# Performance work log

Hardware: AMD Instinct MI355X
Metric: run time of the kernel (lower is better)

Reference implementation:

```python
import jax, jax.numpy as jnp
import numpy as np

_FIRST_DECODE_ID = 0  # _T5_DECODER_START_TOKEN_ID
B, L, V = 1, 520, 32128
REVIEW_INDEX = 512
LENIENCY = 2


def setup_inputs() -> dict:
    key = jax.random.key(0)
    k1, k2, k3 = jax.random.split(key, 3)
    target_logits = jax.random.normal(k1, (B, L, V), dtype=jnp.float32)
    probs = jax.random.uniform(k2, (B, L, V), dtype=jnp.float32)
    input_ids = jax.random.randint(k3, (B, L), 0, V, dtype=jnp.int64)
    return {
        "target_logits": target_logits,
        "probs": probs,
        "input_ids": input_ids,
        "review_index": REVIEW_INDEX,
        "leniency": LENIENCY,
    }


def reference(target_logits, probs, input_ids, review_index, leniency):
    r = int(review_index)
    L = input_ids.shape[1]
    K = L - r  # number of draft tokens under review

    target_probs = jax.nn.softmax(target_logits, axis=-1)          # (1, L, V)
    argmax_ids = jnp.argmax(target_probs, axis=-1)                  # (1, L)
    first = jnp.full((1, 1), _FIRST_DECODE_ID, dtype=input_ids.dtype)
    target_ids = jnp.concatenate([first, argmax_ids.astype(input_ids.dtype)], axis=-1)[:, r:]  # (1, K+1)
    target_probs_s = target_probs[:, r - 1:, :]                     # (1, K+1, V)
    probs_new = probs[:, r - 1:, :]                                 # (1, K+1, V)
    draft_ids = input_ids[:, r:]                                    # (1, K)

    # verification flags (fused replacement of the python early-exit loop)
    eq = target_ids[:, :K] == draft_ids                             # (1, K)
    tp = jnp.take_along_axis(target_probs_s[:, :K, :], draft_ids[..., None], axis=-1)[..., 0]
    pp = jnp.take_along_axis(probs_new[:, :K, :], draft_ids[..., None], axis=-1)[..., 0]
    lenient = (leniency > 1) & (tp > pp / jnp.float32(leniency))
    accept = eq | lenient                                           # (1, K)
    # n_match = length of leading run of accepts == match_ct in the loop
    n_match = jnp.sum(jnp.cumprod(accept.astype(jnp.int32), axis=-1))

    # id_res: prefix (r) + accepted drafts (n_match) + 1 bonus target token, padded to r+K+1
    pos = jnp.arange(K + 1)
    draft_pad = jnp.pad(draft_ids, ((0, 0), (0, 1)))                # (1, K+1)
    new_ids = jnp.where(pos < n_match, draft_pad[0],
                        jnp.where(pos == n_match, target_ids[0], 0))
    id_res = jnp.concatenate([input_ids[0, :r], new_ids])[None, :]  # (1, r+K+1)

    # prob_res: probs[:, :r] ++ target_probs of accepted positions, zero-padded to r+K
    mask = (jnp.arange(K) < n_match)[:, None]
    new_probs = jnp.where(mask, target_probs_s[0, :K, :], jnp.float32(0.0))
    prob_res = jnp.concatenate([probs[0, :r, :], new_probs], axis=0)[None]  # (1, r+K, V)

    return id_res, prob_res, n_match
```

## Files before the change

kernel.cpp:

```cpp
#include <hip/hip_runtime.h>
#include <hip/hip_bf16.h>


#define NCHUNK 32
#define BLK 256
#define CP_EPT 8

struct Ws {
    float pmax[16][NCHUNK];
    float psum[16][NCHUNK];
    int   pidx[16][NCHUNK];
    float mx[16];
    float sum[16];
    int   amax[16];
    int   n_match;
};

struct MIS { float m; int i; float s; };

__device__ inline MIS mis_merge(MIS a, MIS b) {
    MIS r;
    r.i = (b.m > a.m || (b.m == a.m && b.i < a.i)) ? b.i : a.i;
    r.m = fmaxf(a.m, b.m);
    r.s = 0.0f;
    if (a.s > 0.0f) r.s += a.s * expf(a.m - r.m);
    if (b.s > 0.0f) r.s += b.s * expf(b.m - r.m);
    return r;
}

typedef float f4u __attribute__((ext_vector_type(4), aligned(4)));

__global__ void fused_copy_stats(const float* __restrict__ logits,
                                 const float* __restrict__ probs,
                                 float* __restrict__ out, Ws* __restrict__ ws,
                                 int V, int row0, long long prob_off,
                                 int nCopyBlocks, int blocksPerRow, int nf4) {
    int t = threadIdx.x;

    if ((int)blockIdx.x < nCopyBlocks) {
        int y   = blockIdx.x / blocksPerRow;
        int sub = blockIdx.x % blocksPerRow;
        const float* src = probs + (size_t)y * V;
        float*       dst = out + prob_off + (size_t)y * V;

        if (sub == 0) {
            if (t < 3)       dst[t] = src[t];
            else if (t == 3) dst[V - 1] = src[V - 1];
        }
        int f0 = sub * (BLK * CP_EPT) + t;
        #pragma unroll
        for (int k = 0; k < CP_EPT; k++) {
            int f = f0 + k * BLK;
            if (f < nf4) {
                f4u v = *reinterpret_cast<const f4u*>(src + 3 + 4 * f);
                *reinterpret_cast<float4*>(dst + 3 + 4 * f) =
                    float4{v.x, v.y, v.z, v.w};
            }
        }
        return;
    }

    int idx = blockIdx.x - nCopyBlocks;
    int ch = idx & (NCHUNK - 1);
    int j  = idx / NCHUNK;
    int chunk_elems = V / NCHUNK;
    int cf4 = chunk_elems / 4;
    int cbase = ch * chunk_elems;
    const float4* row = (const float4*)(logits + (size_t)(row0 + j) * V + cbase);

    float m = -INFINITY, s = 0.0f;
    int   mi = 0x7fffffff;
    for (int f = t; f < cf4; f += BLK) {
        float4 v = row[f];
        float vv[4] = {v.x, v.y, v.z, v.w};
        int c = cbase + f * 4;
        #pragma unroll
        for (int u = 0; u < 4; u++) {
            float x = vv[u];
            if (x > m) { s = s * expf(m - x) + 1.0f; m = x; mi = c + u; }
            else       { s += expf(x - m); }
        }
    }

    __shared__ float sm[BLK];
    __shared__ int   si[BLK];
    __shared__ float ss[BLK];
    sm[t] = m; si[t] = mi; ss[t] = s;
    __syncthreads();
    for (int w = BLK >> 1; w > 0; w >>= 1) {
        if (t < w) {
            MIS a = {sm[t], si[t], ss[t]};
            MIS b = {sm[t + w], si[t + w], ss[t + w]};
            MIS rr = mis_merge(a, b);
            sm[t] = rr.m; si[t] = rr.i; ss[t] = rr.s;
        }
        __syncthreads();
    }
    if (t == 0) {
        ws->pmax[j][ch] = sm[0];
        ws->psum[j][ch] = ss[0];
        ws->pidx[j][ch] = si[0];
    }
}

__global__ void accept_kernel(const float* __restrict__ logits, const float* __restrict__ probs,
                              const int* __restrict__ ids, const int* __restrict__ leniency_p,
                              float* __restrict__ out, Ws* __restrict__ ws,
                              int V, int r, int K, long long out_last) {
    __shared__ int s_draft[16];
    __shared__ int s_acc[16];
    __shared__ int s_nm;
    int t = threadIdx.x;

    if (t <= K) {
        MIS acc = {ws->pmax[t][0], ws->pidx[t][0], ws->psum[t][0]};
        for (int c = 1; c < NCHUNK; c++) {
            MIS b = {ws->pmax[t][c], ws->pidx[t][c], ws->psum[t][c]};
            acc = mis_merge(acc, b);
        }
        ws->mx[t] = acc.m; ws->sum[t] = acc.s; ws->amax[t] = acc.i;
    }
    __syncthreads();

    for (int i = t; i < r; i += blockDim.x) out[i] = (float)ids[i];

    if (t < K) {
        int dj = ids[r + t];
        s_draft[t] = dj;
        size_t rowoff = (size_t)(r - 1 + t) * V;
        float tp = expf(logits[rowoff + dj] - ws->mx[t]) / ws->sum[t];
        float pp = probs[rowoff + dj];
        int   len = *leniency_p;
        bool eq      = (ws->amax[t] == dj);
        bool lenient = (len > 1) && (tp > pp / (float)len);
        s_acc[t] = (eq || lenient) ? 1 : 0;
    }
    __syncthreads();

    if (t == 0) {
        int nm = 0;
        for (int j = 0; j < K; j++) { if (s_acc[j]) nm++; else break; }
        s_nm = nm;
        ws->n_match = nm;
        out[out_last] = (float)nm;
    }
    __syncthreads();

    if (t <= K) {
        int pos = t, nm = s_nm, v;
        if (pos < nm)       v = s_draft[pos];
        else if (pos == nm) v = ws->amax[pos];
        else                v = 0;
        out[r + pos] = (float)v;
    }
}

#define TP_EPT 4

__global__ void tail_probs_kernel(const float* __restrict__ logits,
                                  float* __restrict__ out, const Ws* __restrict__ ws,
                                  int V, int r, long long prob_off) {
    int j = blockIdx.y;
    long long ob = prob_off + (long long)(r + j) * V;
    int c0 = blockIdx.x * (BLK * TP_EPT) + threadIdx.x;
    int nm = ws->n_match;

    if (j < nm) {
        const float* lg = logits + (size_t)(r - 1 + j) * V;
        float m   = ws->mx[j];
        float inv = 1.0f / ws->sum[j];
        #pragma unroll
        for (int k = 0; k < TP_EPT; k++) {
            int c = c0 + k * BLK;
            if (c < V) out[ob + c] = expf(lg[c] - m) * inv;
        }
    } else {
        #pragma unroll
        for (int k = 0; k < TP_EPT; k++) {
            int c = c0 + k * BLK;
            if (c < V) out[ob + c] = 0.0f;
        }
    }
}

extern "C" void kernel_launch(void* const* d_in, const int* in_sizes, int n_in,
                              void* d_out, int out_size, void* d_ws, size_t ws_size,
                              hipStream_t stream) {
    const float* logits     = (const float*)d_in[0];
    const float* probs      = (const float*)d_in[1];
    const int*   ids        = (const int*)d_in[2];
    const int*   leniency_p = (const int*)d_in[4];
    float* out = (float*)d_out;
    Ws*    ws  = (Ws*)d_ws;

    const int L = in_sizes[2];
    const int V = in_sizes[0] / L;
    const int r = 512;
    const int K = L - r;
    const long long prob_off = (long long)r + K + 1;
    const long long out_last = (long long)out_size - 1;

    const int nf4 = (V - 4) / 4;
    const int blocksPerRow = (nf4 + BLK * CP_EPT - 1) / (BLK * CP_EPT);
    const int nCopyBlocks  = r * blocksPerRow;
    const int nStatsBlocks = (K + 1) * NCHUNK;

    fused_copy_stats<<<nCopyBlocks + nStatsBlocks, BLK, 0, stream>>>(
        logits, probs, out, ws, V, r - 1, prob_off, nCopyBlocks, blocksPerRow, nf4);

    accept_kernel<<<1, 512, 0, stream>>>(logits, probs, ids, leniency_p, out, ws,
                                         V, r, K, out_last);

    dim3 g3((V + BLK * TP_EPT - 1) / (BLK * TP_EPT), K, 1);
    tail_probs_kernel<<<g3, BLK, 0, stream>>>(logits, out, ws, V, r, prob_off);
}
```

Measured before the change: 34.79 us.

## Merge accept step into tail kernel and grid-stride the probs copy

The single-block accept kernel is folded into the tail-probs kernel. Every tail block now redundantly merges the per-chunk stats and recomputes n_match in shared memory, which removes one launch and the workspace round trip. The probs copy becomes a flat grid-stride loop over the whole prefix with nontemporal stores and a fixed grid of 2048 blocks, replacing per-row blocks. The tail writes are also vectorized as float4 with nontemporal stores. The cost is redundant per-block reductions, and NSTATS is hardcoded for K=8.

```diff
diff --git a/kernel.cpp b/kernel.cpp
--- a/kernel.cpp
+++ b/kernel.cpp
@@ -4,16 +4,14 @@
 
 #define NCHUNK 32
 #define BLK 256
-#define CP_EPT 8
+#define NSTATS ((8 + 1) * NCHUNK)
+#define GRID1 2048
+#define NCOPY (GRID1 - NSTATS - 1)
 
 struct Ws {
     float pmax[16][NCHUNK];
     float psum[16][NCHUNK];
     int   pidx[16][NCHUNK];
-    float mx[16];
-    float sum[16];
-    int   amax[16];
-    int   n_match;
 };
 
 struct MIS { float m; int i; float s; };
@@ -28,110 +26,114 @@
     return r;
 }
 
+typedef float f4  __attribute__((ext_vector_type(4)));
 typedef float f4u __attribute__((ext_vector_type(4), aligned(4)));
 
 __global__ void fused_copy_stats(const float* __restrict__ logits,
                                  const float* __restrict__ probs,
+                                 const int* __restrict__ ids,
                                  float* __restrict__ out, Ws* __restrict__ ws,
-                                 int V, int row0, long long prob_off,
-                                 int nCopyBlocks, int blocksPerRow, int nf4) {
+                                 int V, int r, long long prob_off, int nf4) {
     int t = threadIdx.x;
-
-    if ((int)blockIdx.x < nCopyBlocks) {
-        int y   = blockIdx.x / blocksPerRow;
-        int sub = blockIdx.x % blocksPerRow;
-        const float* src = probs + (size_t)y * V;
-        float*       dst = out + prob_off + (size_t)y * V;
-
-        if (sub == 0) {
-            if (t < 3)       dst[t] = src[t];
-            else if (t == 3) dst[V - 1] = src[V - 1];
-        }
-        int f0 = sub * (BLK * CP_EPT) + t;
-        #pragma unroll
-        for (int k = 0; k < CP_EPT; k++) {
-            int f = f0 + k * BLK;
-            if (f < nf4) {
-                f4u v = *reinterpret_cast<const f4u*>(src + 3 + 4 * f);
-                *reinterpret_cast<float4*>(dst + 3 + 4 * f) =
-                    float4{v.x, v.y, v.z, v.w};
+    int b = blockIdx.x;
+
+    if (b < NCOPY) {
+        const float* src = probs + 3;
+        float*       dst = out + prob_off + 3;
+        for (int i = b * BLK + t; i < nf4; i += NCOPY * BLK) {
+            f4u v = *reinterpret_cast<const f4u*>(src + 4 * (size_t)i);
+            __builtin_nontemporal_store((f4)v, reinterpret_cast<f4*>(dst + 4 * (size_t)i));
+        }
+        return;
+    }
+
+    if (b < NCOPY + NSTATS) {
+        int idx = b - NCOPY;
+        int ch = idx & (NCHUNK - 1);
+        int j  = idx / NCHUNK;
+        int chunk_elems = V / NCHUNK;
+        int cf4 = chunk_elems / 4;
+        int cbase = ch * chunk_elems;
+        const float4* row = (const float4*)(logits + (size_t)(r - 1 + j) * V + cbase);
+
+        float m = -INFINITY, s = 0.0f;
+        int   mi = 0x7fffffff;
+        for (int f = t; f < cf4; f += BLK) {
+            float4 v = row[f];
+            float vv[4] = {v.x, v.y, v.z, v.w};
+            int c = cbase + f * 4;
+            #pragma unroll
+            for (int u = 0; u < 4; u++) {
+                float x = vv[u];
+                if (x > m) { s = s * expf(m - x) + 1.0f; m = x; mi = c + u; }
+                else       { s += expf(x - m); }
             }
         }
+
+        __shared__ float sm[BLK];
+        __shared__ int   si[BLK];
+        __shared__ float ss[BLK];
+        sm[t] = m; si[t] = mi; ss[t] = s;
+        __syncthreads();
+        for (int w = BLK >> 1; w > 0; w >>= 1) {
+            if (t < w) {
+                MIS a = {sm[t], si[t], ss[t]};
+                MIS bb = {sm[t + w], si[t + w], ss[t + w]};
+                MIS rr = mis_merge(a, bb);
+                sm[t] = rr.m; si[t] = rr.i; ss[t] = rr.s;
+            }
+            __syncthreads();
+        }
+        if (t == 0) {
+            ws->pmax[j][ch] = sm[0];
+            ws->psum[j][ch] = ss[0];
+            ws->pidx[j][ch] = si[0];
+        }
         return;
     }
 
-    int idx = blockIdx.x - nCopyBlocks;
-    int ch = idx & (NCHUNK - 1);
-    int j  = idx / NCHUNK;
-    int chunk_elems = V / NCHUNK;
-    int cf4 = chunk_elems / 4;
-    int cbase = ch * chunk_elems;
-    const float4* row = (const float4*)(logits + (size_t)(row0 + j) * V + cbase);
-
-    float m = -INFINITY, s = 0.0f;
-    int   mi = 0x7fffffff;
-    for (int f = t; f < cf4; f += BLK) {
-        float4 v = row[f];
-        float vv[4] = {v.x, v.y, v.z, v.w};
-        int c = cbase + f * 4;
-        #pragma unroll
-        for (int u = 0; u < 4; u++) {
-            float x = vv[u];
-            if (x > m) { s = s * expf(m - x) + 1.0f; m = x; mi = c + u; }
-            else       { s += expf(x - m); }
-        }
-    }
-
-    __shared__ float sm[BLK];
-    __shared__ int   si[BLK];
-    __shared__ float ss[BLK];
-    sm[t] = m; si[t] = mi; ss[t] = s;
-    __syncthreads();
-    for (int w = BLK >> 1; w > 0; w >>= 1) {
-        if (t < w) {
-            MIS a = {sm[t], si[t], ss[t]};
-            MIS b = {sm[t + w], si[t + w], ss[t + w]};
-            MIS rr = mis_merge(a, b);
-            sm[t] = rr.m; si[t] = rr.i; ss[t] = rr.s;
-        }
-        __syncthreads();
-    }
-    if (t == 0) {
-        ws->pmax[j][ch] = sm[0];
-        ws->psum[j][ch] = ss[0];
-        ws->pidx[j][ch] = si[0];
-    }
-}
-
-__global__ void accept_kernel(const float* __restrict__ logits, const float* __restrict__ probs,
-                              const int* __restrict__ ids, const int* __restrict__ leniency_p,
-                              float* __restrict__ out, Ws* __restrict__ ws,
-                              int V, int r, int K, long long out_last) {
-    __shared__ int s_draft[16];
-    __shared__ int s_acc[16];
-    __shared__ int s_nm;
+    for (int i = t; i < r; i += BLK) out[i] = (float)ids[i];
+    if (t < 3)       out[prob_off + t] = probs[t];
+    else if (t == 3) {
+        long long last = (long long)r * V - 1;
+        out[prob_off + last] = probs[last];
+    }
+}
+
+#define TP_EPT 8
+
+__global__ void tail_kernel(const float* __restrict__ logits, const float* __restrict__ probs,
+                            const int* __restrict__ ids, const int* __restrict__ leniency_p,
+                            float* __restrict__ out, const Ws* __restrict__ ws,
+                            int V, int r, int K, long long prob_off, long long out_last) {
+    __shared__ float s_mx[12];
+    __shared__ float s_sum[12];
+    __shared__ int   s_amax[12];
+    __shared__ int   s_draft[12];
+    __shared__ int   s_acc[12];
+    __shared__ int   s_nm;
     int t = threadIdx.x;
+    int j   = blockIdx.y;
+    int sub = blockIdx.x;
 
     if (t <= K) {
         MIS acc = {ws->pmax[t][0], ws->pidx[t][0], ws->psum[t][0]};
         for (int c = 1; c < NCHUNK; c++) {
-            MIS b = {ws->pmax[t][c], ws->pidx[t][c], ws->psum[t][c]};
-            acc = mis_merge(acc, b);
-        }
-        ws->mx[t] = acc.m; ws->sum[t] = acc.s; ws->amax[t] = acc.i;
+            MIS bb = {ws->pmax[t][c], ws->pidx[t][c], ws->psum[t][c]};
+            acc = mis_merge(acc, bb);
+        }
+        s_mx[t] = acc.m; s_sum[t] = acc.s; s_amax[t] = acc.i;
     }
     __syncthreads();
-
-    for (int i = t; i < r; i += blockDim.x) out[i] = (float)ids[i];
 
     if (t < K) {
         int dj = ids[r + t];
         s_draft[t] = dj;
         size_t rowoff = (size_t)(r - 1 + t) * V;
-        float tp = expf(logits[rowoff + dj] - ws->mx[t]) / ws->sum[t];
+        float tp = expf(logits[rowoff + dj] - s_mx[t]) / s_sum[t];
         float pp = probs[rowoff + dj];
         int   len = *leniency_p;
-        bool eq      = (ws->amax[t] == dj);
+        bool eq      = (s_amax[t] == dj);
         bool lenient = (len > 1) && (tp > pp / (float)len);
         s_acc[t] = (eq || lenient) ? 1 : 0;
     }
@@ -139,46 +141,49 @@
 
     if (t == 0) {
         int nm = 0;
-        for (int j = 0; j < K; j++) { if (s_acc[j]) nm++; else break; }
+        for (int q = 0; q < K; q++) { if (s_acc[q]) nm++; else break; }
         s_nm = nm;
-        ws->n_match = nm;
-        out[out_last] = (float)nm;
     }
     __syncthreads();
-
-    if (t <= K) {
-        int pos = t, nm = s_nm, v;
-        if (pos < nm)       v = s_draft[pos];
-        else if (pos == nm) v = ws->amax[pos];
-        else                v = 0;
-        out[r + pos] = (float)v;
-    }
-}
-
-#define TP_EPT 4
-
-__global__ void tail_probs_kernel(const float* __restrict__ logits,
-                                  float* __restrict__ out, const Ws* __restrict__ ws,
-                                  int V, int r, long long prob_off) {
-    int j = blockIdx.y;
+    int nm = s_nm;
+
+    if (j == 0 && sub == 0) {
+        if (t <= K) {
+            int v;
+            if (t < nm)       v = s_draft[t];
+            else if (t == nm) v = s_amax[t];
+            else              v = 0;
+            out[r + t] = (float)v;
+        }
+        if (t == K + 1) out[out_last] = (float)nm;
+    }
+
     long long ob = prob_off + (long long)(r + j) * V;
-    int c0 = blockIdx.x * (BLK * TP_EPT) + threadIdx.x;
-    int nm = ws->n_match;
-
-    if (j < nm) {
-        const float* lg = logits + (size_t)(r - 1 + j) * V;
-        float m   = ws->mx[j];
-        float inv = 1.0f / ws->sum[j];
-        #pragma unroll
-        for (int k = 0; k < TP_EPT; k++) {
-            int c = c0 + k * BLK;
-            if (c < V) out[ob + c] = expf(lg[c] - m) * inv;
-        }
-    } else {
-        #pragma unroll
-        for (int k = 0; k < TP_EPT; k++) {
-            int c = c0 + k * BLK;
-            if (c < V) out[ob + c] = 0.0f;
+    const float* lg = logits + (size_t)(r - 1 + j) * V;
+    bool on = (j < nm);
+    float m   = s_mx[j];
+    float inv = on ? (1.0f / s_sum[j]) : 0.0f;
+
+    if (sub == 0) {
+        if (t < 3)       out[ob + t]     = on ? expf(lg[t] - m) * inv : 0.0f;
+        else if (t == 3) out[ob + V - 1] = on ? expf(lg[V - 1] - m) * inv : 0.0f;
+    }
+    int nf4r = (V - 4) / 4;
+    float* dst = out + ob + 3;
+    const float* srcl = lg + 3;
+    #pragma unroll
+    for (int k = 0; k < TP_EPT; k++) {
+        int i = sub * (BLK * TP_EPT) + t + k * BLK;
+        if (i < nf4r) {
+            f4 v;
+            if (on) {
+                f4u x = *reinterpret_cast<const f4u*>(srcl + 4 * (size_t)i);
+                v.x = expf(x.x - m) * inv; v.y = expf(x.y - m) * inv;
+                v.z = expf(x.z - m) * inv; v.w = expf(x.w - m) * inv;
+            } else {
+                v = (f4)0.0f;
+            }
+            __builtin_nontemporal_store(v, reinterpret_cast<f4*>(dst + 4 * (size_t)i));
         }
     }
 }
@@ -200,17 +205,13 @@
     const long long prob_off = (long long)r + K + 1;
     const long long out_last = (long long)out_size - 1;
 
-    const int nf4 = (V - 4) / 4;
-    const int blocksPerRow = (nf4 + BLK * CP_EPT - 1) / (BLK * CP_EPT);
-    const int nCopyBlocks  = r * blocksPerRow;
-    const int nStatsBlocks = (K + 1) * NCHUNK;
-
-    fused_copy_stats<<<nCopyBlocks + nStatsBlocks, BLK, 0, stream>>>(
-        logits, probs, out, ws, V, r - 1, prob_off, nCopyBlocks, blocksPerRow, nf4);
-
-    accept_kernel<<<1, 512, 0, stream>>>(logits, probs, ids, leniency_p, out, ws,
-                                         V, r, K, out_last);
-
-    dim3 g3((V + BLK * TP_EPT - 1) / (BLK * TP_EPT), K, 1);
-    tail_probs_kernel<<<g3, BLK, 0, stream>>>(logits, out, ws, V, r, prob_off);
-}
+    const long long N = (long long)r * V;
+    const int nf4 = (int)((N - 3) / 4);
+
+    fused_copy_stats<<<GRID1, BLK, 0, stream>>>(logits, probs, ids, out, ws,
+                                                V, r, prob_off, nf4);
+
+    dim3 g2((V / 4 + BLK * TP_EPT - 1) / (BLK * TP_EPT), K, 1);
+    tail_kernel<<<g2, BLK, 0, stream>>>(logits, probs, ids, leniency_p, out, ws,
+                                        V, r, K, prob_off, out_last);
+}
```

Result: faster. 33.71 us (-3.1%).
